# Kernel optimization log

Hardware: AMD Instinct MI355X
Metric: run time of the kernel (lower is better)

Reference implementation:

```python
import jax, jax.numpy as jnp
import numpy as np
import math

IN_C, OUT_C, KH, KW = 128, 128, 3, 3
GROUPS_NUM, NUM_W = 8, 8
STRIDE, PAD, DIL = 1, 1, 1
BETA = 1.0


def setup_inputs() -> dict:
    key = jax.random.key(0)
    ks = jax.random.split(key, 6)
    B, H, W = 8, 56, 56
    n = IN_C * KH * KW
    bound = math.sqrt(6.0 / n)  # reset_parameters bound for weight templates
    inputs = jax.random.normal(ks[0], (B, IN_C, H, W), jnp.float32)
    mask = jax.random.randint(ks[1], (B, H, W), 0, GROUPS_NUM)
    Alpha = jax.random.uniform(ks[2], (B, GROUPS_NUM, H, W), jnp.float32)
    weight_templates = jax.random.uniform(ks[3], (OUT_C * IN_C * KH * KW, NUM_W), jnp.float32, -bound, bound)
    routing_w = jax.random.normal(ks[4], (GROUPS_NUM * NUM_W, IN_C), jnp.float32) * 0.01
    routing_b = jnp.zeros((GROUPS_NUM * NUM_W,), jnp.float32)
    bias = jnp.zeros((OUT_C,), jnp.float32)
    return dict(inputs=inputs, mask=mask, Alpha=Alpha, weight_templates=weight_templates,
                routing_w=routing_w, routing_b=routing_b, bias=bias, use_alpha=1)


def _unfold(x):
    # torch F.unfold-compatible im2col: [B, C*KH*KW, Ho, Wo], channel-major feature order
    return jax.lax.conv_general_dilated_patches(
        x, (KH, KW), (STRIDE, STRIDE), [(PAD, PAD), (PAD, PAD)],
        rhs_dilation=(DIL, DIL), dimension_numbers=('NCHW', 'OIHW', 'NCHW'))


def reference(inputs, mask, Alpha, weight_templates, routing_w, routing_b, bias, use_alpha):
    B, C, H, W = inputs.shape
    K = IN_C * KH * KW
    # SE-style routing: GAP -> fc -> scaled sigmoid (alpha=1.0 in source)
    x_se = inputs.reshape(B, C, -1).mean(-1)                              # [B, C]
    x_se = 2.0 * jax.nn.sigmoid(x_se @ routing_w.T + routing_b) / NUM_W   # [B, G*num_W]
    # blend weight templates: F.linear(x_se.reshape(-1,num_W), weight)
    w = x_se.reshape(B * GROUPS_NUM, NUM_W) @ weight_templates.T          # [B*G, O*K]
    w = w.reshape(B, GROUPS_NUM, OUT_C, K).transpose(0, 2, 3, 1)          # [B, O, K, G]
    patches = _unfold(inputs)                                             # [B, K, Ho, Wo]
    # per-group convolution outputs, then per-pixel group routing
    y = jnp.einsum('bokg,bkhw->boghw', w, patches)                        # [B, O, G, Ho, Wo]
    if use_alpha:
        probs = jax.nn.softmax(BETA * Alpha, axis=1)                      # soft routing [B, G, Ho, Wo]
    else:
        probs = jax.nn.one_hot(mask, GROUPS_NUM, axis=1, dtype=y.dtype)   # hard per-pixel group select
    out = jnp.einsum('boghw,bghw->bohw', y, probs)
    return out + bias.reshape(1, -1, 1, 1)
```

## Files before the change

### kernel.cpp

```cpp
#include <hip/hip_runtime.h>
#include <stdint.h>

#define IN_C   128
#define OUT_C  128
#define KTOT   1152
#define NG     8
#define NW     8
#define NB     8
#define HH     56
#define WWID   56
#define NPIX   3136
#define PPAD   3200
#define MTOT   1024
#define HALO   58
#define HPIX   (HALO*HALO)


typedef __attribute__((ext_vector_type(8))) short short8;
typedef __attribute__((ext_vector_type(8))) unsigned short ushort8;
typedef __attribute__((ext_vector_type(4))) float f32x4;

__device__ __forceinline__ unsigned short f2bf(float f) {
    unsigned u = __float_as_uint(f);
    u += 0x7FFF + ((u >> 16) & 1);
    return (unsigned short)(u >> 16);
}

__device__ __forceinline__ void cp16(const unsigned short* g, unsigned short* l) {
    __builtin_amdgcn_global_load_lds(
        (const __attribute__((address_space(1))) unsigned int*)g,
        (__attribute__((address_space(3))) unsigned int*)l,
        16, 0, 0);
}

__global__ __launch_bounds__(256) void prep_kernel(const float* __restrict__ in,
                                                   const float* __restrict__ T,
                                                   float* __restrict__ xse,
                                                   unsigned short* __restrict__ Apack,
                                                   unsigned short* __restrict__ Xt) {
    __shared__ __align__(16) unsigned char smem[32768];
    const int blk = blockIdx.x;
    const int t = threadIdx.x;

    if (blk < 1024) {
        const float* src = in + (size_t)blk * NPIX;
        float s = 0.f;
        for (int i = t; i < NPIX / 4; i += 256) {
            float4 v = ((const float4*)src)[i];
            s += v.x + v.y + v.z + v.w;
        }
        #pragma unroll
        for (int off = 32; off; off >>= 1) s += __shfl_down(s, off);
        float* ws4 = (float*)smem;
        if ((t & 63) == 0) ws4[t >> 6] = s;
        __syncthreads();
        if (t == 0)
            xse[blk] = (ws4[0] + ws4[1] + ws4[2] + ws4[3]) * (1.0f / (float)NPIX);
        return;
    }
    if (blk < 1152) {
        unsigned short* lh = (unsigned short*)smem;
        const int o = blk - 1024;
        const float* To = T + (size_t)o * 9216;
        #pragma unroll
        for (int it = 0; it < 9; it++) {
            const int f = it * 256 + t;
            const float4 v = ((const float4*)To)[f];
            ushort4 h;
            h.x = f2bf(v.x); h.y = f2bf(v.y); h.z = f2bf(v.z); h.w = f2bf(v.w);
            *(ushort4*)&lh[f * 4] = h;
        }
        __syncthreads();
        const int m16b = o >> 1;
        const int lrb = (o & 1) * 8;
        #pragma unroll
        for (int it = 0; it < 5; it++) {
            const int ch = it * 256 + t;
            if (ch < 1152) {
                const int j = ch & 7, kc = ch >> 3;
                const int s = kc >> 4, c0 = (kc & 15) << 3;
                const int kt = kc >> 2, lq = kc & 3;
                ushort8 v;
                #pragma unroll
                for (int i = 0; i < 8; i++)
                    v[i] = lh[((c0 + i) * 9 + s) * 8 + j];
                const size_t off = ((((size_t)m16b * 36 + kt) * 4 + lq) * 16 + lrb + j) * 8;
                *(ushort8*)&Apack[off] = v;
            }
        }
        return;
    }
    unsigned short* tile = (unsigned short*)smem;
    const int idx = blk - 1152;
    const int yt = idx % 28;
    const int b  = idx / 28;
    const int y0 = yt * 2;

    #pragma unroll
    for (int it = 0; it < 14; it++) {
        const int f = it * 256 + t;
        const int c = f / 28;
        const int rem = f - c * 28;
        const int y = rem / 14;
        const int x4 = rem - y * 14;
        const float4 v = *(const float4*)(in + ((size_t)(b * IN_C + c)) * NPIX
                                          + (y0 + y) * WWID + x4 * 4);
        unsigned short bf0 = f2bf(v.x), bf1 = f2bf(v.y), bf2 = f2bf(v.z), bf3 = f2bf(v.w);
        const int ppb = (y * WWID + x4 * 4) ^ (((c >> 3) & 15) << 2);
        uint2 pk;
        pk.x = (unsigned)bf0 | ((unsigned)bf1 << 16);
        pk.y = (unsigned)bf2 | ((unsigned)bf3 << 16);
        *(uint2*)&tile[c * 128 + ppb] = pk;
    }
    __syncthreads();

    #pragma unroll
    for (int it = 0; it < 7; it++) {
        const int ch = it * 256 + t;
        const int oct = ch & 15;
        const int pp = ch >> 4;
        const int sw = oct << 2;
        ushort8 v;
        #pragma unroll
        for (int i = 0; i < 8; i++)
            v[i] = tile[(oct * 8 + i) * 128 + (pp ^ sw)];
        const int y2 = (pp >= WWID) ? 1 : 0;
        const int xg = pp - y2 * WWID;
        const size_t hp = (size_t)b * HPIX + (y0 + y2 + 1) * HALO + (xg + 1);
        *(ushort8*)&Xt[hp * 128 + oct * 8] = v;
    }

    if (t < 64) {
        const int pi = t >> 4, oct = t & 15;
        const int yy = y0 + 1 + (pi >> 1);
        const int xx = (pi & 1) * 57;
        *(ushort8*)&Xt[((size_t)b * HPIX + yy * HALO + xx) * 128 + oct * 8] =
            (ushort8){0, 0, 0, 0, 0, 0, 0, 0};
    }
    if (yt == 0 || yt == 27) {
        const int yy = (yt == 0) ? 0 : 57;
        #pragma unroll
        for (int it = 0; it < 4; it++) {
            const int ch = it * 256 + t;
            if (ch < 928) {
                const int xx = ch >> 4, oct = ch & 15;
                *(ushort8*)&Xt[((size_t)b * HPIX + yy * HALO + xx) * 128 + oct * 8] =
                    (ushort8){0, 0, 0, 0, 0, 0, 0, 0};
            }
        }
    }
}

__global__ __launch_bounds__(256) void s_kernel(const float* __restrict__ Alpha,
                                                const int* __restrict__ mask,
                                                const float* __restrict__ xse,
                                                const float* __restrict__ rw,
                                                const float* __restrict__ rb,
                                                const int* __restrict__ use_alpha,
                                                float* __restrict__ Sws) {
    const int b = blockIdx.y;
    const int t = threadIdx.x;
    const int p = blockIdx.x * 256 + t;
    __shared__ float xs[IN_C];
    __shared__ float rsh[64];
    if (t < IN_C) xs[t] = xse[b * IN_C + t];
    __syncthreads();
    if (t < 64) {
        float acc = rb[t];
        #pragma unroll 8
        for (int c = 0; c < IN_C; c++) acc += xs[c] * rw[t * IN_C + c];
        rsh[t] = 0.25f / (1.0f + expf(-acc));
    }
    __syncthreads();
    if (p >= PPAD) return;
    float sj[8] = {0, 0, 0, 0, 0, 0, 0, 0};
    if (p < NPIX) {
        float pr[8];
        if (use_alpha[0]) {
            float a[8], m = -1e30f;
            #pragma unroll
            for (int g = 0; g < 8; g++) {
                a[g] = Alpha[((size_t)(b * NG + g)) * NPIX + p];
                m = fmaxf(m, a[g]);
            }
            float sum = 0.f;
            #pragma unroll
            for (int g = 0; g < 8; g++) { pr[g] = expf(a[g] - m); sum += pr[g]; }
            float inv = 1.f / sum;
            #pragma unroll
            for (int g = 0; g < 8; g++) pr[g] *= inv;
        } else {
            int mg = mask[(size_t)b * NPIX + p];
            #pragma unroll
            for (int g = 0; g < 8; g++) pr[g] = (g == mg) ? 1.f : 0.f;
        }
        #pragma unroll
        for (int g = 0; g < 8; g++)
            #pragma unroll
            for (int j = 0; j < 8; j++) sj[j] += pr[g] * rsh[g * 8 + j];
    }
    float* dst = Sws + ((size_t)b * PPAD + p) * 8;
    *(f32x4*)dst = (f32x4){sj[0], sj[1], sj[2], sj[3]};
    *(f32x4*)(dst + 4) = (f32x4){sj[4], sj[5], sj[6], sj[7]};
}

__global__ __launch_bounds__(256) void gemm_kernel(const unsigned short* __restrict__ Apack,
                                                   const unsigned short* __restrict__ Xt,
                                                   const float* __restrict__ Sws,
                                                   const float* __restrict__ bias,
                                                   float* __restrict__ out) {
    __shared__ __align__(16) unsigned short Bsh[4][512 * 8];
    const int tid = threadIdx.x;
    const int wv = tid >> 6, ln = tid & 63;
    const int lq = ln >> 4, lr = ln & 15;
    const int wrow = wv >> 1, wcol = wv & 1;

    const int lid = blockIdx.x;
    const int b   = lid & 7;
    const int sl  = lid >> 3;
    const int mt  = sl & 15;
    const int nt  = sl >> 4;

    f32x4 acc[2][4];
    #pragma unroll
    for (int i = 0; i < 2; i++)
        #pragma unroll
        for (int j = 0; j < 4; j++) acc[i][j] = (f32x4){0.f, 0.f, 0.f, 0.f};

    const int js = tid & 3;
    const int r0 = tid >> 2,  q0 = js ^ (r0 & 3) ^ ((r0 >> 2) & 3);
    const int r1 = r0 + 64,   q1 = js ^ (r1 & 3) ^ ((r1 >> 2) & 3);
    const int p0 = min(nt * 128 + r0, NPIX - 1);
    const int p1 = min(nt * 128 + r1, NPIX - 1);
    const int y0p = p0 / WWID, x0p = p0 - y0p * WWID;
    const int y1p = p1 / WWID, x1p = p1 - y1p * WWID;
    const unsigned short* gb0 = Xt + ((size_t)b * HPIX + y0p * HALO + x0p) * 128 + q0 * 8;
    const unsigned short* gb1 = Xt + ((size_t)b * HPIX + y1p * HALO + x1p) * 128 + q1 * 8;
    unsigned short* lbA[4];
    #pragma unroll
    for (int i = 0; i < 4; i++) lbA[i] = &Bsh[i][(wv * 64) * 8];

    const unsigned short* gaw[2];
    #pragma unroll
    for (int tm = 0; tm < 2; tm++) {
        const int m16 = mt * 4 + wrow * 2 + tm;
        gaw[tm] = Apack + ((size_t)m16 * 36 * 64 + ln) * 8;
    }

    const int jj = lq ^ (lr & 3) ^ ((lr >> 2) & 3);

    cp16(gb0, lbA[0]); cp16(gb1, lbA[0] + 256 * 8);
    cp16(gb0 + 32, lbA[1]); cp16(gb1 + 32, lbA[1] + 256 * 8);
    short8 afc[2][2], afn[2][2];
    #pragma unroll
    for (int tm = 0; tm < 2; tm++) afc[0][tm] = *(const short8*)(gaw[tm]);
    #pragma unroll
    for (int tm = 0; tm < 2; tm++) afc[1][tm] = *(const short8*)(gaw[tm] + 512);

    #pragma unroll 1
    for (int it = 0; it < 9; it++) {
        __syncthreads();
        {
            const int st2 = it * 4 + 2, st3 = it * 4 + 3;
            const int nk2 = st2 * 32, s2 = nk2 >> 7;
            const int kh2 = s2 / 3, kw2 = s2 - 3 * kh2;
            const int off2 = (kh2 * HALO + kw2) * 128 + (nk2 & 127);
            const int nk3 = st3 * 32, s3 = nk3 >> 7;
            const int kh3 = s3 / 3, kw3 = s3 - 3 * kh3;
            const int off3 = (kh3 * HALO + kw3) * 128 + (nk3 & 127);
            cp16(gb0 + off2, lbA[2]); cp16(gb1 + off2, lbA[2] + 256 * 8);
            cp16(gb0 + off3, lbA[3]); cp16(gb1 + off3, lbA[3] + 256 * 8);
            #pragma unroll
            for (int tm = 0; tm < 2; tm++)
                afn[0][tm] = *(const short8*)(gaw[tm] + (size_t)st2 * 512);
            #pragma unroll
            for (int tm = 0; tm < 2; tm++)
                afn[1][tm] = *(const short8*)(gaw[tm] + (size_t)st3 * 512);
            __builtin_amdgcn_sched_barrier(0);

            {
                short8 bfr[4];
                #pragma unroll
                for (int tn = 0; tn < 4; tn++) {
                    const int row = wcol * 64 + tn * 16 + lr;
                    bfr[tn] = *(const short8*)&Bsh[0][(row * 4 + jj) * 8];
                }
                #pragma unroll
                for (int tm = 0; tm < 2; tm++)
                    #pragma unroll
                    for (int tn = 0; tn < 4; tn++)
                        acc[tm][tn] = __builtin_amdgcn_mfma_f32_16x16x32_bf16(
                            afc[0][tm], bfr[tn], acc[tm][tn], 0, 0, 0);
            }
            {
                short8 bfr[4];
                #pragma unroll
                for (int tn = 0; tn < 4; tn++) {
                    const int row = wcol * 64 + tn * 16 + lr;
                    bfr[tn] = *(const short8*)&Bsh[1][(row * 4 + jj) * 8];
                }
                #pragma unroll
                for (int tm = 0; tm < 2; tm++)
                    #pragma unroll
                    for (int tn = 0; tn < 4; tn++)
                        acc[tm][tn] = __builtin_amdgcn_mfma_f32_16x16x32_bf16(
                            afc[1][tm], bfr[tn], acc[tm][tn], 0, 0, 0);
            }
        }
        __syncthreads();
        {
            if (it < 8) {
                const int st2 = it * 4 + 4, st3 = it * 4 + 5;
                const int nk2 = st2 * 32, s2 = nk2 >> 7;
                const int kh2 = s2 / 3, kw2 = s2 - 3 * kh2;
                const int off2 = (kh2 * HALO + kw2) * 128 + (nk2 & 127);
                const int nk3 = st3 * 32, s3 = nk3 >> 7;
                const int kh3 = s3 / 3, kw3 = s3 - 3 * kh3;
                const int off3 = (kh3 * HALO + kw3) * 128 + (nk3 & 127);
                cp16(gb0 + off2, lbA[0]); cp16(gb1 + off2, lbA[0] + 256 * 8);
                cp16(gb0 + off3, lbA[1]); cp16(gb1 + off3, lbA[1] + 256 * 8);
                #pragma unroll
                for (int tm = 0; tm < 2; tm++)
                    afc[0][tm] = *(const short8*)(gaw[tm] + (size_t)st2 * 512);
                #pragma unroll
                for (int tm = 0; tm < 2; tm++)
                    afc[1][tm] = *(const short8*)(gaw[tm] + (size_t)st3 * 512);
            }
            __builtin_amdgcn_sched_barrier(0);

            {
                short8 bfr[4];
                #pragma unroll
                for (int tn = 0; tn < 4; tn++) {
                    const int row = wcol * 64 + tn * 16 + lr;
                    bfr[tn] = *(const short8*)&Bsh[2][(row * 4 + jj) * 8];
                }
                #pragma unroll
                for (int tm = 0; tm < 2; tm++)
                    #pragma unroll
                    for (int tn = 0; tn < 4; tn++)
                        acc[tm][tn] = __builtin_amdgcn_mfma_f32_16x16x32_bf16(
                            afn[0][tm], bfr[tn], acc[tm][tn], 0, 0, 0);
            }
            {
                short8 bfr[4];
                #pragma unroll
                for (int tn = 0; tn < 4; tn++) {
                    const int row = wcol * 64 + tn * 16 + lr;
                    bfr[tn] = *(const short8*)&Bsh[3][(row * 4 + jj) * 8];
                }
                #pragma unroll
                for (int tm = 0; tm < 2; tm++)
                    #pragma unroll
                    for (int tn = 0; tn < 4; tn++)
                        acc[tm][tn] = __builtin_amdgcn_mfma_f32_16x16x32_bf16(
                            afn[1][tm], bfr[tn], acc[tm][tn], 0, 0, 0);
            }
        }
    }

    const int j0 = (lq & 1) * 4;
    const int oo = lq >> 1;
    #pragma unroll
    for (int tm = 0; tm < 2; tm++) {
        const int o = mt * 8 + wrow * 4 + tm * 2 + oo;
        const float bo = bias[o];
        #pragma unroll
        for (int tn = 0; tn < 4; tn++) {
            const int p = nt * 128 + wcol * 64 + tn * 16 + lr;
            const f32x4 sv = *(const f32x4*)&Sws[((size_t)b * PPAD + p) * 8 + j0];
            const f32x4 a = acc[tm][tn];
            float part = a.x * sv.x + a.y * sv.y + a.z * sv.z + a.w * sv.w;
            float tot = part + __shfl_xor(part, 16);
            if ((lq & 1) == 0 && p < NPIX)
                out[((size_t)b * OUT_C + o) * NPIX + p] = tot + bo;
        }
    }
}

extern "C" void kernel_launch(void* const* d_in, const int* in_sizes, int n_in,
                              void* d_out, int out_size, void* d_ws, size_t ws_size,
                              hipStream_t stream) {
    const float* inputs = (const float*)d_in[0];
    const int*   mask   = (const int*)d_in[1];
    const float* Alpha  = (const float*)d_in[2];
    const float* wtmpl  = (const float*)d_in[3];
    const float* rw     = (const float*)d_in[4];
    const float* rb     = (const float*)d_in[5];
    const float* bias   = (const float*)d_in[6];
    const int*   ua     = (const int*)d_in[7];
    float* out = (float*)d_out;

    char* ws = (char*)d_ws;
    unsigned short* Xt  = (unsigned short*)ws;
    unsigned short* Apk = (unsigned short*)(ws + 6889472);
    float*          Sws = (float*)(ws + 9248768);
    float*          xse = (float*)(ws + 10067968);

    prep_kernel<<<1376, 256, 0, stream>>>(inputs, wtmpl, xse, Apk, Xt);
    s_kernel<<<dim3(13, NB), 256, 0, stream>>>(Alpha, mask, xse, rw, rb, ua, Sws);
    gemm_kernel<<<3200, 256, 0, stream>>>(Apk, Xt, Sws, bias, out);
}
```

Baseline: 161.2 us.

## Enlarge GEMM block tile to 128x256 with 512 threads per block

```diff
diff --git a/kernel.cpp b/kernel.cpp
--- a/kernel.cpp
+++ b/kernel.cpp
@@ -204,12 +204,12 @@
     *(f32x4*)(dst + 4) = (f32x4){sj[4], sj[5], sj[6], sj[7]};
 }
 
-__global__ __launch_bounds__(256) void gemm_kernel(const unsigned short* __restrict__ Apack,
-                                                   const unsigned short* __restrict__ Xt,
-                                                   const float* __restrict__ Sws,
-                                                   const float* __restrict__ bias,
-                                                   float* __restrict__ out) {
-    __shared__ __align__(16) unsigned short Bsh[4][512 * 8];
+__global__ __launch_bounds__(512, 4) void gemm_kernel(const unsigned short* __restrict__ Apack,
+                                                      const unsigned short* __restrict__ Xt,
+                                                      const float* __restrict__ Sws,
+                                                      const float* __restrict__ bias,
+                                                      float* __restrict__ out) {
+    __shared__ __align__(16) unsigned short Bsh[4][1024 * 8];
     const int tid = threadIdx.x;
     const int wv = tid >> 6, ln = tid & 63;
     const int lq = ln >> 4, lr = ln & 15;
@@ -218,20 +218,20 @@
     const int lid = blockIdx.x;
     const int b   = lid & 7;
     const int sl  = lid >> 3;
-    const int mt  = sl & 15;
-    const int nt  = sl >> 4;
-
-    f32x4 acc[2][4];
+    const int mt  = sl & 7;
+    const int nt  = sl >> 3;
+
+    f32x4 acc[2][8];
     #pragma unroll
     for (int i = 0; i < 2; i++)
         #pragma unroll
-        for (int j = 0; j < 4; j++) acc[i][j] = (f32x4){0.f, 0.f, 0.f, 0.f};
+        for (int j = 0; j < 8; j++) acc[i][j] = (f32x4){0.f, 0.f, 0.f, 0.f};
 
     const int js = tid & 3;
     const int r0 = tid >> 2,  q0 = js ^ (r0 & 3) ^ ((r0 >> 2) & 3);
-    const int r1 = r0 + 64,   q1 = js ^ (r1 & 3) ^ ((r1 >> 2) & 3);
-    const int p0 = min(nt * 128 + r0, NPIX - 1);
-    const int p1 = min(nt * 128 + r1, NPIX - 1);
+    const int r1 = r0 + 128,  q1 = js ^ (r1 & 3) ^ ((r1 >> 2) & 3);
+    const int p0 = min(nt * 256 + r0, NPIX - 1);
+    const int p1 = min(nt * 256 + r1, NPIX - 1);
     const int y0p = p0 / WWID, x0p = p0 - y0p * WWID;
     const int y1p = p1 / WWID, x1p = p1 - y1p * WWID;
     const unsigned short* gb0 = Xt + ((size_t)b * HPIX + y0p * HALO + x0p) * 128 + q0 * 8;
@@ -243,14 +243,14 @@
     const unsigned short* gaw[2];
     #pragma unroll
     for (int tm = 0; tm < 2; tm++) {
-        const int m16 = mt * 4 + wrow * 2 + tm;
+        const int m16 = mt * 8 + wrow * 2 + tm;
         gaw[tm] = Apack + ((size_t)m16 * 36 * 64 + ln) * 8;
     }
 
     const int jj = lq ^ (lr & 3) ^ ((lr >> 2) & 3);
 
-    cp16(gb0, lbA[0]); cp16(gb1, lbA[0] + 256 * 8);
-    cp16(gb0 + 32, lbA[1]); cp16(gb1 + 32, lbA[1] + 256 * 8);
+    cp16(gb0, lbA[0]); cp16(gb1, lbA[0] + 512 * 8);
+    cp16(gb0 + 32, lbA[1]); cp16(gb1 + 32, lbA[1] + 512 * 8);
     short8 afc[2][2], afn[2][2];
     #pragma unroll
     for (int tm = 0; tm < 2; tm++) afc[0][tm] = *(const short8*)(gaw[tm]);
@@ -268,8 +268,8 @@
             const int nk3 = st3 * 32, s3 = nk3 >> 7;
             const int kh3 = s3 / 3, kw3 = s3 - 3 * kh3;
             const int off3 = (kh3 * HALO + kw3) * 128 + (nk3 & 127);
-            cp16(gb0 + off2, lbA[2]); cp16(gb1 + off2, lbA[2] + 256 * 8);
-            cp16(gb0 + off3, lbA[3]); cp16(gb1 + off3, lbA[3] + 256 * 8);
+            cp16(gb0 + off2, lbA[2]); cp16(gb1 + off2, lbA[2] + 512 * 8);
+            cp16(gb0 + off3, lbA[3]); cp16(gb1 + off3, lbA[3] + 512 * 8);
             #pragma unroll
             for (int tm = 0; tm < 2; tm++)
                 afn[0][tm] = *(const short8*)(gaw[tm] + (size_t)st2 * 512);
@@ -278,33 +278,35 @@
                 afn[1][tm] = *(const short8*)(gaw[tm] + (size_t)st3 * 512);
             __builtin_amdgcn_sched_barrier(0);
 
-            {
+            #pragma unroll
+            for (int hf = 0; hf < 2; hf++) {
                 short8 bfr[4];
                 #pragma unroll
                 for (int tn = 0; tn < 4; tn++) {
-                    const int row = wcol * 64 + tn * 16 + lr;
+                    const int row = wcol * 128 + hf * 64 + tn * 16 + lr;
                     bfr[tn] = *(const short8*)&Bsh[0][(row * 4 + jj) * 8];
                 }
                 #pragma unroll
                 for (int tm = 0; tm < 2; tm++)
                     #pragma unroll
                     for (int tn = 0; tn < 4; tn++)
-                        acc[tm][tn] = __builtin_amdgcn_mfma_f32_16x16x32_bf16(
-                            afc[0][tm], bfr[tn], acc[tm][tn], 0, 0, 0);
-            }
-            {
+                        acc[tm][hf * 4 + tn] = __builtin_amdgcn_mfma_f32_16x16x32_bf16(
+                            afc[0][tm], bfr[tn], acc[tm][hf * 4 + tn], 0, 0, 0);
+            }
+            #pragma unroll
+            for (int hf = 0; hf < 2; hf++) {
                 short8 bfr[4];
                 #pragma unroll
                 for (int tn = 0; tn < 4; tn++) {
-                    const int row = wcol * 64 + tn * 16 + lr;
+                    const int row = wcol * 128 + hf * 64 + tn * 16 + lr;
                     bfr[tn] = *(const short8*)&Bsh[1][(row * 4 + jj) * 8];
                 }
                 #pragma unroll
                 for (int tm = 0; tm < 2; tm++)
                     #pragma unroll
                     for (int tn = 0; tn < 4; tn++)
-                        acc[tm][tn] = __builtin_amdgcn_mfma_f32_16x16x32_bf16(
-                            afc[1][tm], bfr[tn], acc[tm][tn], 0, 0, 0);
+                        acc[tm][hf * 4 + tn] = __builtin_amdgcn_mfma_f32_16x16x32_bf16(
+                            afc[1][tm], bfr[tn], acc[tm][hf * 4 + tn], 0, 0, 0);
             }
         }
         __syncthreads();
@@ -317,8 +319,8 @@
                 const int nk3 = st3 * 32, s3 = nk3 >> 7;
                 const int kh3 = s3 / 3, kw3 = s3 - 3 * kh3;
                 const int off3 = (kh3 * HALO + kw3) * 128 + (nk3 & 127);
-                cp16(gb0 + off2, lbA[0]); cp16(gb1 + off2, lbA[0] + 256 * 8);
-                cp16(gb0 + off3, lbA[1]); cp16(gb1 + off3, lbA[1] + 256 * 8);
+                cp16(gb0 + off2, lbA[0]); cp16(gb1 + off2, lbA[0] + 512 * 8);
+                cp16(gb0 + off3, lbA[1]); cp16(gb1 + off3, lbA[1] + 512 * 8);
                 #pragma unroll
                 for (int tm = 0; tm < 2; tm++)
                     afc[0][tm] = *(const short8*)(gaw[tm] + (size_t)st2 * 512);
@@ -328,33 +330,35 @@
             }
             __builtin_amdgcn_sched_barrier(0);
 
-            {
+            #pragma unroll
+            for (int hf = 0; hf < 2; hf++) {
                 short8 bfr[4];
                 #pragma unroll
                 for (int tn = 0; tn < 4; tn++) {
-                    const int row = wcol * 64 + tn * 16 + lr;
+                    const int row = wcol * 128 + hf * 64 + tn * 16 + lr;
                     bfr[tn] = *(const short8*)&Bsh[2][(row * 4 + jj) * 8];
                 }
                 #pragma unroll
                 for (int tm = 0; tm < 2; tm++)
                     #pragma unroll
                     for (int tn = 0; tn < 4; tn++)
-                        acc[tm][tn] = __builtin_amdgcn_mfma_f32_16x16x32_bf16(
-                            afn[0][tm], bfr[tn], acc[tm][tn], 0, 0, 0);
-            }
-            {
+                        acc[tm][hf * 4 + tn] = __builtin_amdgcn_mfma_f32_16x16x32_bf16(
+                            afn[0][tm], bfr[tn], acc[tm][hf * 4 + tn], 0, 0, 0);
+            }
+            #pragma unroll
+            for (int hf = 0; hf < 2; hf++) {
                 short8 bfr[4];
                 #pragma unroll
                 for (int tn = 0; tn < 4; tn++) {
-                    const int row = wcol * 64 + tn * 16 + lr;
+                    const int row = wcol * 128 + hf * 64 + tn * 16 + lr;
                     bfr[tn] = *(const short8*)&Bsh[3][(row * 4 + jj) * 8];
                 }
                 #pragma unroll
                 for (int tm = 0; tm < 2; tm++)
                     #pragma unroll
                     for (int tn = 0; tn < 4; tn++)
-                        acc[tm][tn] = __builtin_amdgcn_mfma_f32_16x16x32_bf16(
-                            afn[1][tm], bfr[tn], acc[tm][tn], 0, 0, 0);
+                        acc[tm][hf * 4 + tn] = __builtin_amdgcn_mfma_f32_16x16x32_bf16(
+                            afn[1][tm], bfr[tn], acc[tm][hf * 4 + tn], 0, 0, 0);
             }
         }
     }
@@ -363,13 +367,14 @@
     const int oo = lq >> 1;
     #pragma unroll
     for (int tm = 0; tm < 2; tm++) {
-        const int o = mt * 8 + wrow * 4 + tm * 2 + oo;
+        const int o = mt * 16 + wrow * 4 + tm * 2 + oo;
         const float bo = bias[o];
         #pragma unroll
-        for (int tn = 0; tn < 4; tn++) {
-            const int p = nt * 128 + wcol * 64 + tn * 16 + lr;
-            const f32x4 sv = *(const f32x4*)&Sws[((size_t)b * PPAD + p) * 8 + j0];
-            const f32x4 a = acc[tm][tn];
+        for (int tn8 = 0; tn8 < 8; tn8++) {
+            const int p = nt * 256 + wcol * 128 + tn8 * 16 + lr;
+            const int pS = min(p, NPIX - 1);
+            const f32x4 sv = *(const f32x4*)&Sws[((size_t)b * PPAD + pS) * 8 + j0];
+            const f32x4 a = acc[tm][tn8];
             float part = a.x * sv.x + a.y * sv.y + a.z * sv.z + a.w * sv.w;
             float tot = part + __shfl_xor(part, 16);
             if ((lq & 1) == 0 && p < NPIX)
@@ -399,5 +404,5 @@
 
     prep_kernel<<<1376, 256, 0, stream>>>(inputs, wtmpl, xse, Apk, Xt);
     s_kernel<<<dim3(13, NB), 256, 0, stream>>>(Alpha, mask, xse, rw, rb, ua, Sws);
-    gemm_kernel<<<3200, 256, 0, stream>>>(Apk, Xt, Sws, bias, out);
-}
+    gemm_kernel<<<832, 512, 0, stream>>>(Apk, Xt, Sws, bias, out);
+}
```

Result: slower. 214.7 us (+33.2%).

## Fuse routing/softmax weight computation into GEMM epilogue, drop s_kernel

Applied to the files above, without the earlier changes.

```diff
diff --git a/kernel.cpp b/kernel.cpp
--- a/kernel.cpp
+++ b/kernel.cpp
@@ -151,62 +151,14 @@
     }
 }
 
-__global__ __launch_bounds__(256) void s_kernel(const float* __restrict__ Alpha,
-                                                const int* __restrict__ mask,
-                                                const float* __restrict__ xse,
-                                                const float* __restrict__ rw,
-                                                const float* __restrict__ rb,
-                                                const int* __restrict__ use_alpha,
-                                                float* __restrict__ Sws) {
-    const int b = blockIdx.y;
-    const int t = threadIdx.x;
-    const int p = blockIdx.x * 256 + t;
-    __shared__ float xs[IN_C];
-    __shared__ float rsh[64];
-    if (t < IN_C) xs[t] = xse[b * IN_C + t];
-    __syncthreads();
-    if (t < 64) {
-        float acc = rb[t];
-        #pragma unroll 8
-        for (int c = 0; c < IN_C; c++) acc += xs[c] * rw[t * IN_C + c];
-        rsh[t] = 0.25f / (1.0f + expf(-acc));
-    }
-    __syncthreads();
-    if (p >= PPAD) return;
-    float sj[8] = {0, 0, 0, 0, 0, 0, 0, 0};
-    if (p < NPIX) {
-        float pr[8];
-        if (use_alpha[0]) {
-            float a[8], m = -1e30f;
-            #pragma unroll
-            for (int g = 0; g < 8; g++) {
-                a[g] = Alpha[((size_t)(b * NG + g)) * NPIX + p];
-                m = fmaxf(m, a[g]);
-            }
-            float sum = 0.f;
-            #pragma unroll
-            for (int g = 0; g < 8; g++) { pr[g] = expf(a[g] - m); sum += pr[g]; }
-            float inv = 1.f / sum;
-            #pragma unroll
-            for (int g = 0; g < 8; g++) pr[g] *= inv;
-        } else {
-            int mg = mask[(size_t)b * NPIX + p];
-            #pragma unroll
-            for (int g = 0; g < 8; g++) pr[g] = (g == mg) ? 1.f : 0.f;
-        }
-        #pragma unroll
-        for (int g = 0; g < 8; g++)
-            #pragma unroll
-            for (int j = 0; j < 8; j++) sj[j] += pr[g] * rsh[g * 8 + j];
-    }
-    float* dst = Sws + ((size_t)b * PPAD + p) * 8;
-    *(f32x4*)dst = (f32x4){sj[0], sj[1], sj[2], sj[3]};
-    *(f32x4*)(dst + 4) = (f32x4){sj[4], sj[5], sj[6], sj[7]};
-}
-
 __global__ __launch_bounds__(256) void gemm_kernel(const unsigned short* __restrict__ Apack,
                                                    const unsigned short* __restrict__ Xt,
-                                                   const float* __restrict__ Sws,
+                                                   const float* __restrict__ Alpha,
+                                                   const int* __restrict__ mask,
+                                                   const float* __restrict__ xse,
+                                                   const float* __restrict__ rw,
+                                                   const float* __restrict__ rb,
+                                                   const int* __restrict__ use_alpha,
                                                    const float* __restrict__ bias,
                                                    float* __restrict__ out) {
     __shared__ __align__(16) unsigned short Bsh[4][512 * 8];
@@ -359,7 +311,57 @@
         }
     }
 
+    float accr = rb[ln];
+    {
+        const float* xsb = xse + b * IN_C;
+        const float* rwr = rw + ln * IN_C;
+        #pragma unroll 8
+        for (int c = 0; c < IN_C; c += 4) {
+            const f32x4 xv = *(const f32x4*)&xsb[c];
+            const f32x4 wv = *(const f32x4*)&rwr[c];
+            accr += xv.x * wv.x + xv.y * wv.y + xv.z * wv.z + xv.w * wv.w;
+        }
+    }
+    const float rln = 0.25f / (1.0f + expf(-accr));
+
     const int j0 = (lq & 1) * 4;
+    const int ua = use_alpha[0];
+    f32x4 sv[4];
+    #pragma unroll
+    for (int tn = 0; tn < 4; tn++) {
+        const int p = nt * 128 + wcol * 64 + tn * 16 + lr;
+        const int pS = min(p, NPIX - 1);
+        float pr[8];
+        if (ua) {
+            float a[8], m = -1e30f;
+            #pragma unroll
+            for (int g = 0; g < 8; g++) {
+                a[g] = Alpha[((size_t)(b * NG + g)) * NPIX + pS];
+                m = fmaxf(m, a[g]);
+            }
+            float sum = 0.f;
+            #pragma unroll
+            for (int g = 0; g < 8; g++) { pr[g] = expf(a[g] - m); sum += pr[g]; }
+            const float inv = 1.f / sum;
+            #pragma unroll
+            for (int g = 0; g < 8; g++) pr[g] *= inv;
+        } else {
+            const int mg = mask[(size_t)b * NPIX + pS];
+            #pragma unroll
+            for (int g = 0; g < 8; g++) pr[g] = (g == mg) ? 1.f : 0.f;
+        }
+        f32x4 sj = (f32x4){0.f, 0.f, 0.f, 0.f};
+        #pragma unroll
+        for (int g = 0; g < 8; g++) {
+            const int base = g * 8 + j0;
+            sj.x += pr[g] * __shfl(rln, base + 0);
+            sj.y += pr[g] * __shfl(rln, base + 1);
+            sj.z += pr[g] * __shfl(rln, base + 2);
+            sj.w += pr[g] * __shfl(rln, base + 3);
+        }
+        sv[tn] = sj;
+    }
+
     const int oo = lq >> 1;
     #pragma unroll
     for (int tm = 0; tm < 2; tm++) {
@@ -368,9 +370,9 @@
         #pragma unroll
         for (int tn = 0; tn < 4; tn++) {
             const int p = nt * 128 + wcol * 64 + tn * 16 + lr;
-            const f32x4 sv = *(const f32x4*)&Sws[((size_t)b * PPAD + p) * 8 + j0];
             const f32x4 a = acc[tm][tn];
-            float part = a.x * sv.x + a.y * sv.y + a.z * sv.z + a.w * sv.w;
+            const f32x4 s = sv[tn];
+            float part = a.x * s.x + a.y * s.y + a.z * s.z + a.w * s.w;
             float tot = part + __shfl_xor(part, 16);
             if ((lq & 1) == 0 && p < NPIX)
                 out[((size_t)b * OUT_C + o) * NPIX + p] = tot + bo;
@@ -394,10 +396,8 @@
     char* ws = (char*)d_ws;
     unsigned short* Xt  = (unsigned short*)ws;
     unsigned short* Apk = (unsigned short*)(ws + 6889472);
-    float*          Sws = (float*)(ws + 9248768);
     float*          xse = (float*)(ws + 10067968);
 
     prep_kernel<<<1376, 256, 0, stream>>>(inputs, wtmpl, xse, Apk, Xt);
-    s_kernel<<<dim3(13, NB), 256, 0, stream>>>(Alpha, mask, xse, rw, rb, ua, Sws);
-    gemm_kernel<<<3200, 256, 0, stream>>>(Apk, Xt, Sws, bias, out);
+    gemm_kernel<<<3200, 256, 0, stream>>>(Apk, Xt, Alpha, mask, xse, rw, rb, ua, bias, out);
 }
```

After: 226.6 us. 1.41x slower.
